# Performance work log

Measured on AMD Instinct MI355X. Metric: run time of the kernel, lower is better.

Reference implementation:

```python
import jax, jax.numpy as jnp
import numpy as np

N_FILTERS = 8   # K
N_SIMPLICES = 8192  # N (rows/cols of Laplacian)
BATCH = 64      # B
FEAT = 128      # F

def setup_inputs() -> dict:
    key = jax.random.key(0)
    k1, k2, k3 = jax.random.split(key, 3)
    x = jax.random.normal(k1, (BATCH, N_SIMPLICES, FEAT), dtype=jnp.float32)
    L = jax.random.normal(k2, (N_SIMPLICES, N_SIMPLICES), dtype=jnp.float32)
    # filter_weights: K vectors of length N, init N(0, 0.01) in the original
    W = 0.01 * jax.random.normal(k3, (N_FILTERS, N_SIMPLICES), dtype=jnp.float32)
    return {"x": x, "L": L, "W": W}

def reference(x, L, W):
    # Original per filter k: act( sum_n w_k[n] * (L @ x[b])[n, f] )
    # = act( (w_k^T L) @ x[b] ).  Fuse diag(w)@Lx + sum into wL = W @ L.
    wL = jnp.matmul(W, L)                       # [K, N]
    out = jnp.einsum('kn,bnf->kbf', wL, x)      # [K, B, F]
    return jnp.tanh(out)                        # stacked version of the K-output list
```

## Files before the change

kernel.cpp:

```cpp
#include <hip/hip_runtime.h>
#include <math.h>

#define N_SIMP 8192
#define K_FILT 8
#define BATCH  64
#define FEAT   128
#define MCHUNK 64
#define NCHUNK 64


__global__ __launch_bounds__(256) void wl_partial_kernel(const float* __restrict__ W,
                                                         const float* __restrict__ L,
                                                         float* __restrict__ pL) {
    const int ntile = blockIdx.x & 7;
    const int mc    = blockIdx.x >> 3;
    const int n0    = ntile * 1024;
    const int m0    = mc * 128;

    __shared__ float Ws[K_FILT][128];
    for (int idx = threadIdx.x; idx < K_FILT * 128; idx += 256) {
        int k = idx >> 7, j = idx & 127;
        Ws[k][j] = W[k * N_SIMP + m0 + j];
    }
    __syncthreads();

    const int n = n0 + threadIdx.x * 4;
    float4 acc[K_FILT];
#pragma unroll
    for (int k = 0; k < K_FILT; k++) acc[k] = make_float4(0.f, 0.f, 0.f, 0.f);

    const float* Lp = L + (size_t)m0 * N_SIMP + n;
    for (int j0 = 0; j0 < 128; j0 += 4) {
        float4 l0 = *(const float4*)(Lp);
        float4 l1 = *(const float4*)(Lp + N_SIMP);
        float4 l2 = *(const float4*)(Lp + 2 * N_SIMP);
        float4 l3 = *(const float4*)(Lp + 3 * N_SIMP);
        Lp += 4 * N_SIMP;
#pragma unroll
        for (int k = 0; k < K_FILT; k++) {
            float w0 = Ws[k][j0], w1 = Ws[k][j0 + 1], w2 = Ws[k][j0 + 2], w3 = Ws[k][j0 + 3];
            acc[k].x += w0 * l0.x; acc[k].y += w0 * l0.y; acc[k].z += w0 * l0.z; acc[k].w += w0 * l0.w;
            acc[k].x += w1 * l1.x; acc[k].y += w1 * l1.y; acc[k].z += w1 * l1.z; acc[k].w += w1 * l1.w;
            acc[k].x += w2 * l2.x; acc[k].y += w2 * l2.y; acc[k].z += w2 * l2.z; acc[k].w += w2 * l2.w;
            acc[k].x += w3 * l3.x; acc[k].y += w3 * l3.y; acc[k].z += w3 * l3.z; acc[k].w += w3 * l3.w;
        }
    }

#pragma unroll
    for (int k = 0; k < K_FILT; k++)
        *(float4*)&pL[(size_t)(mc * K_FILT + k) * N_SIMP + n] = acc[k];
}

__global__ __launch_bounds__(256) void wl_reduce_kernel(const float* __restrict__ pL,
                                                        float* __restrict__ wL) {
    const int i4 = (blockIdx.x * 256 + threadIdx.x) * 4;
    float4 s = make_float4(0.f, 0.f, 0.f, 0.f);
#pragma unroll 4
    for (int mc = 0; mc < MCHUNK; mc++) {
        float4 v = *(const float4*)&pL[(size_t)mc * (K_FILT * N_SIMP) + i4];
        s.x += v.x; s.y += v.y; s.z += v.z; s.w += v.w;
    }
    *(float4*)&wL[i4] = s;
}

__global__ __launch_bounds__(64) void conv_partial_kernel(const float* __restrict__ wL,
                                                          const float* __restrict__ x,
                                                          float* __restrict__ pO) {
    const int nc   = blockIdx.x & 63;
    const int b    = blockIdx.x >> 6;
    const int n0   = nc * 128;
    const int lane = threadIdx.x;
    const int f0   = (lane & 31) * 4;
    const int nl   = lane >> 5;

    __shared__ float wls[K_FILT][128];
    for (int idx = lane; idx < K_FILT * 128; idx += 64) {
        int k = idx >> 7, j = idx & 127;
        wls[k][j] = wL[k * N_SIMP + n0 + j];
    }
    __syncthreads();

    float4 acc[K_FILT];
#pragma unroll
    for (int k = 0; k < K_FILT; k++) acc[k] = make_float4(0.f, 0.f, 0.f, 0.f);

    const float* xp = x + (size_t)b * N_SIMP * FEAT + (size_t)(n0 + nl) * FEAT + f0;
    for (int j0 = 0; j0 < 128; j0 += 8) {
        float4 x0 = *(const float4*)(xp);
        float4 x1 = *(const float4*)(xp + 2 * FEAT);
        float4 x2 = *(const float4*)(xp + 4 * FEAT);
        float4 x3 = *(const float4*)(xp + 6 * FEAT);
        xp += 8 * FEAT;
#pragma unroll
        for (int k = 0; k < K_FILT; k++) {
            float w0 = wls[k][j0 + 0 + nl];
            float w1 = wls[k][j0 + 2 + nl];
            float w2 = wls[k][j0 + 4 + nl];
            float w3 = wls[k][j0 + 6 + nl];
            acc[k].x += w0 * x0.x; acc[k].y += w0 * x0.y; acc[k].z += w0 * x0.z; acc[k].w += w0 * x0.w;
            acc[k].x += w1 * x1.x; acc[k].y += w1 * x1.y; acc[k].z += w1 * x1.z; acc[k].w += w1 * x1.w;
            acc[k].x += w2 * x2.x; acc[k].y += w2 * x2.y; acc[k].z += w2 * x2.z; acc[k].w += w2 * x2.w;
            acc[k].x += w3 * x3.x; acc[k].y += w3 * x3.y; acc[k].z += w3 * x3.z; acc[k].w += w3 * x3.w;
        }
    }

#pragma unroll
    for (int k = 0; k < K_FILT; k++) {
        acc[k].x += __shfl_xor(acc[k].x, 32);
        acc[k].y += __shfl_xor(acc[k].y, 32);
        acc[k].z += __shfl_xor(acc[k].z, 32);
        acc[k].w += __shfl_xor(acc[k].w, 32);
    }

    if (nl == 0) {
#pragma unroll
        for (int k = 0; k < K_FILT; k++)
            *(float4*)&pO[((size_t)(nc * K_FILT + k) * BATCH + b) * FEAT + f0] = acc[k];
    }
}

__global__ __launch_bounds__(256) void conv_reduce_kernel(const float* __restrict__ pO,
                                                          float* __restrict__ out) {
    const int i4 = (blockIdx.x * 256 + threadIdx.x) * 4;
    float4 s = make_float4(0.f, 0.f, 0.f, 0.f);
#pragma unroll 4
    for (int nc = 0; nc < NCHUNK; nc++) {
        float4 v = *(const float4*)&pO[(size_t)nc * (K_FILT * BATCH * FEAT) + i4];
        s.x += v.x; s.y += v.y; s.z += v.z; s.w += v.w;
    }
    float4 r;
    r.x = tanhf(s.x); r.y = tanhf(s.y); r.z = tanhf(s.z); r.w = tanhf(s.w);
    *(float4*)&out[i4] = r;
}

__global__ void zero_ws_kernel(float* __restrict__ p, int n) {
    int i = blockIdx.x * blockDim.x + threadIdx.x;
    if (i < n) p[i] = 0.0f;
}

__global__ __launch_bounds__(256) void wl_atomic_kernel(const float* __restrict__ W,
                                                        const float* __restrict__ L,
                                                        float* __restrict__ wL) {
    const int ntile = blockIdx.x & 7;
    const int mc    = blockIdx.x >> 3;
    const int n0    = ntile * 1024;
    const int m0    = mc * 128;
    __shared__ float Ws[K_FILT][128];
    for (int idx = threadIdx.x; idx < K_FILT * 128; idx += 256) {
        int k = idx >> 7, j = idx & 127;
        Ws[k][j] = W[k * N_SIMP + m0 + j];
    }
    __syncthreads();
    const int n = n0 + threadIdx.x * 4;
    float4 acc[K_FILT];
#pragma unroll
    for (int k = 0; k < K_FILT; k++) acc[k] = make_float4(0.f, 0.f, 0.f, 0.f);
    const float* Lp = L + (size_t)m0 * N_SIMP + n;
    for (int j = 0; j < 128; j++) {
        float4 lv = *(const float4*)Lp;
        Lp += N_SIMP;
#pragma unroll
        for (int k = 0; k < K_FILT; k++) {
            float w = Ws[k][j];
            acc[k].x += w * lv.x; acc[k].y += w * lv.y; acc[k].z += w * lv.z; acc[k].w += w * lv.w;
        }
    }
#pragma unroll
    for (int k = 0; k < K_FILT; k++) {
        float* dst = &wL[k * N_SIMP + n];
        atomicAdd(dst + 0, acc[k].x); atomicAdd(dst + 1, acc[k].y);
        atomicAdd(dst + 2, acc[k].z); atomicAdd(dst + 3, acc[k].w);
    }
}

__global__ __launch_bounds__(64) void conv_atomic_kernel(const float* __restrict__ wL,
                                                         const float* __restrict__ x,
                                                         float* __restrict__ out_acc) {
    const int nc   = blockIdx.x & 63;
    const int b    = blockIdx.x >> 6;
    const int n0   = nc * 128;
    const int lane = threadIdx.x;
    const int f0   = (lane & 31) * 4;
    const int nl   = lane >> 5;
    __shared__ float wls[K_FILT][128];
    for (int idx = lane; idx < K_FILT * 128; idx += 64) {
        int k = idx >> 7, j = idx & 127;
        wls[k][j] = wL[k * N_SIMP + n0 + j];
    }
    __syncthreads();
    float4 acc[K_FILT];
#pragma unroll
    for (int k = 0; k < K_FILT; k++) acc[k] = make_float4(0.f, 0.f, 0.f, 0.f);
    const float* xp = x + (size_t)b * N_SIMP * FEAT + (size_t)(n0 + nl) * FEAT + f0;
    for (int jj = 0; jj < 64; jj++) {
        int j = jj * 2 + nl;
        float4 xv = *(const float4*)xp;
        xp += 2 * FEAT;
#pragma unroll
        for (int k = 0; k < K_FILT; k++) {
            float w = wls[k][j];
            acc[k].x += w * xv.x; acc[k].y += w * xv.y; acc[k].z += w * xv.z; acc[k].w += w * xv.w;
        }
    }
#pragma unroll
    for (int k = 0; k < K_FILT; k++) {
        acc[k].x += __shfl_xor(acc[k].x, 32);
        acc[k].y += __shfl_xor(acc[k].y, 32);
        acc[k].z += __shfl_xor(acc[k].z, 32);
        acc[k].w += __shfl_xor(acc[k].w, 32);
    }
    if (nl == 0) {
#pragma unroll
        for (int k = 0; k < K_FILT; k++) {
            float* dst = &out_acc[((size_t)k * BATCH + b) * FEAT + f0];
            atomicAdd(dst + 0, acc[k].x); atomicAdd(dst + 1, acc[k].y);
            atomicAdd(dst + 2, acc[k].z); atomicAdd(dst + 3, acc[k].w);
        }
    }
}

__global__ void tanh_kernel(const float* __restrict__ acc, float* __restrict__ out) {
    int i = blockIdx.x * blockDim.x + threadIdx.x;
    if (i < K_FILT * BATCH * FEAT) out[i] = tanhf(acc[i]);
}

extern "C" void kernel_launch(void* const* d_in, const int* in_sizes, int n_in,
                              void* d_out, int out_size, void* d_ws, size_t ws_size,
                              hipStream_t stream) {
    const float* x = (const float*)d_in[0];
    const float* L = (const float*)d_in[1];
    const float* W = (const float*)d_in[2];
    float* out = (float*)d_out;

    const size_t partial_elems = (size_t)MCHUNK * K_FILT * N_SIMP;
    const size_t need = (partial_elems + K_FILT * N_SIMP) * sizeof(float);

    if (ws_size >= need) {
        float* partials = (float*)d_ws;
        float* wL       = partials + partial_elems;

        wl_partial_kernel<<<8 * MCHUNK, 256, 0, stream>>>(W, L, partials);
        wl_reduce_kernel<<<64, 256, 0, stream>>>(partials, wL);
        conv_partial_kernel<<<BATCH * NCHUNK, 64, 0, stream>>>(wL, x, partials);
        conv_reduce_kernel<<<64, 256, 0, stream>>>(partials, out);
    } else {
        float* wL      = (float*)d_ws;
        float* out_acc = wL + (size_t)K_FILT * N_SIMP;
        const int n_zero = K_FILT * N_SIMP + K_FILT * BATCH * FEAT;
        zero_ws_kernel<<<(n_zero + 255) / 256, 256, 0, stream>>>(wL, n_zero);
        wl_atomic_kernel<<<512, 256, 0, stream>>>(W, L, wL);
        conv_atomic_kernel<<<BATCH * 64, 64, 0, stream>>>(wL, x, out_acc);
        tanh_kernel<<<(K_FILT * BATCH * FEAT + 255) / 256, 256, 0, stream>>>(out_acc, out);
    }
}
```

Baseline: 516.3 us.

## Software-prefetch L and x loads and split reductions across more blocks

The wL partial kernel now loads eight rows of L at a time and prefetches the next eight while computing on the current ones. The conv partial kernel gets the same double-buffered prefetch of x rows. Both reduction kernels are replaced by one templated reduce that splits the 64 partial chunks across four thread groups per block, combines them through shared memory, and launches 256 blocks instead of 64 to raise parallelism. The prefetching raises register pressure, which may lower occupancy.

```diff
diff --git a/kernel.cpp b/kernel.cpp
--- a/kernel.cpp
+++ b/kernel.cpp
@@ -30,19 +30,37 @@
     for (int k = 0; k < K_FILT; k++) acc[k] = make_float4(0.f, 0.f, 0.f, 0.f);
 
     const float* Lp = L + (size_t)m0 * N_SIMP + n;
-    for (int j0 = 0; j0 < 128; j0 += 4) {
-        float4 l0 = *(const float4*)(Lp);
-        float4 l1 = *(const float4*)(Lp + N_SIMP);
-        float4 l2 = *(const float4*)(Lp + 2 * N_SIMP);
-        float4 l3 = *(const float4*)(Lp + 3 * N_SIMP);
-        Lp += 4 * N_SIMP;
-#pragma unroll
-        for (int k = 0; k < K_FILT; k++) {
-            float w0 = Ws[k][j0], w1 = Ws[k][j0 + 1], w2 = Ws[k][j0 + 2], w3 = Ws[k][j0 + 3];
-            acc[k].x += w0 * l0.x; acc[k].y += w0 * l0.y; acc[k].z += w0 * l0.z; acc[k].w += w0 * l0.w;
-            acc[k].x += w1 * l1.x; acc[k].y += w1 * l1.y; acc[k].z += w1 * l1.z; acc[k].w += w1 * l1.w;
-            acc[k].x += w2 * l2.x; acc[k].y += w2 * l2.y; acc[k].z += w2 * l2.z; acc[k].w += w2 * l2.w;
-            acc[k].x += w3 * l3.x; acc[k].y += w3 * l3.y; acc[k].z += w3 * l3.z; acc[k].w += w3 * l3.w;
+
+    float4 c[8];
+#pragma unroll
+    for (int r = 0; r < 8; r++) c[r] = *(const float4*)(Lp + (size_t)r * N_SIMP);
+    Lp += 8 * (size_t)N_SIMP;
+
+    for (int j0 = 0; j0 < 120; j0 += 8) {
+        float4 nx[8];
+#pragma unroll
+        for (int r = 0; r < 8; r++) nx[r] = *(const float4*)(Lp + (size_t)r * N_SIMP);
+        Lp += 8 * (size_t)N_SIMP;
+
+#pragma unroll
+        for (int k = 0; k < K_FILT; k++) {
+#pragma unroll
+            for (int r = 0; r < 8; r++) {
+                float w = Ws[k][j0 + r];
+                acc[k].x += w * c[r].x; acc[k].y += w * c[r].y;
+                acc[k].z += w * c[r].z; acc[k].w += w * c[r].w;
+            }
+        }
+#pragma unroll
+        for (int r = 0; r < 8; r++) c[r] = nx[r];
+    }
+#pragma unroll
+    for (int k = 0; k < K_FILT; k++) {
+#pragma unroll
+        for (int r = 0; r < 8; r++) {
+            float w = Ws[k][120 + r];
+            acc[k].x += w * c[r].x; acc[k].y += w * c[r].y;
+            acc[k].z += w * c[r].z; acc[k].w += w * c[r].w;
         }
     }
 
@@ -51,16 +69,36 @@
         *(float4*)&pL[(size_t)(mc * K_FILT + k) * N_SIMP + n] = acc[k];
 }
 
-__global__ __launch_bounds__(256) void wl_reduce_kernel(const float* __restrict__ pL,
-                                                        float* __restrict__ wL) {
-    const int i4 = (blockIdx.x * 256 + threadIdx.x) * 4;
+template <bool TANH>
+__global__ __launch_bounds__(256) void reduce64_kernel(const float* __restrict__ p,
+                                                       float* __restrict__ out) {
+    const int t  = threadIdx.x & 63;
+    const int g  = threadIdx.x >> 6;
+    const int i4 = blockIdx.x * 256 + t * 4;
+
+    const float* base = p + (size_t)(g * 16) * 65536 + i4;
     float4 s = make_float4(0.f, 0.f, 0.f, 0.f);
-#pragma unroll 4
-    for (int mc = 0; mc < MCHUNK; mc++) {
-        float4 v = *(const float4*)&pL[(size_t)mc * (K_FILT * N_SIMP) + i4];
+#pragma unroll
+    for (int mc = 0; mc < 16; mc++) {
+        float4 v = *(const float4*)(base + (size_t)mc * 65536);
         s.x += v.x; s.y += v.y; s.z += v.z; s.w += v.w;
     }
-    *(float4*)&wL[i4] = s;
+
+    __shared__ float4 red[4][64];
+    red[g][t] = s;
+    __syncthreads();
+
+    if (g == 0) {
+        float4 a = red[1][t], b = red[2][t], c = red[3][t];
+        s.x += a.x + b.x + c.x;
+        s.y += a.y + b.y + c.y;
+        s.z += a.z + b.z + c.z;
+        s.w += a.w + b.w + c.w;
+        if (TANH) {
+            s.x = tanhf(s.x); s.y = tanhf(s.y); s.z = tanhf(s.z); s.w = tanhf(s.w);
+        }
+        *(float4*)&out[i4] = s;
+    }
 }
 
 __global__ __launch_bounds__(64) void conv_partial_kernel(const float* __restrict__ wL,
@@ -84,13 +122,8 @@
 #pragma unroll
     for (int k = 0; k < K_FILT; k++) acc[k] = make_float4(0.f, 0.f, 0.f, 0.f);
 
-    const float* xp = x + (size_t)b * N_SIMP * FEAT + (size_t)(n0 + nl) * FEAT + f0;
-    for (int j0 = 0; j0 < 128; j0 += 8) {
-        float4 x0 = *(const float4*)(xp);
-        float4 x1 = *(const float4*)(xp + 2 * FEAT);
-        float4 x2 = *(const float4*)(xp + 4 * FEAT);
-        float4 x3 = *(const float4*)(xp + 6 * FEAT);
-        xp += 8 * FEAT;
+    auto compute = [&](int j0, const float4& x0, const float4& x1,
+                       const float4& x2, const float4& x3) {
 #pragma unroll
         for (int k = 0; k < K_FILT; k++) {
             float w0 = wls[k][j0 + 0 + nl];
@@ -102,7 +135,25 @@
             acc[k].x += w2 * x2.x; acc[k].y += w2 * x2.y; acc[k].z += w2 * x2.z; acc[k].w += w2 * x2.w;
             acc[k].x += w3 * x3.x; acc[k].y += w3 * x3.y; acc[k].z += w3 * x3.z; acc[k].w += w3 * x3.w;
         }
-    }
+    };
+
+    const float* xp = x + (size_t)b * N_SIMP * FEAT + (size_t)(n0 + nl) * FEAT + f0;
+    float4 c0 = *(const float4*)(xp);
+    float4 c1 = *(const float4*)(xp + 2 * FEAT);
+    float4 c2 = *(const float4*)(xp + 4 * FEAT);
+    float4 c3 = *(const float4*)(xp + 6 * FEAT);
+    xp += 8 * FEAT;
+
+    for (int j0 = 0; j0 < 120; j0 += 8) {
+        float4 p0 = *(const float4*)(xp);
+        float4 p1 = *(const float4*)(xp + 2 * FEAT);
+        float4 p2 = *(const float4*)(xp + 4 * FEAT);
+        float4 p3 = *(const float4*)(xp + 6 * FEAT);
+        xp += 8 * FEAT;
+        compute(j0, c0, c1, c2, c3);
+        c0 = p0; c1 = p1; c2 = p2; c3 = p3;
+    }
+    compute(120, c0, c1, c2, c3);
 
 #pragma unroll
     for (int k = 0; k < K_FILT; k++) {
@@ -117,20 +168,6 @@
         for (int k = 0; k < K_FILT; k++)
             *(float4*)&pO[((size_t)(nc * K_FILT + k) * BATCH + b) * FEAT + f0] = acc[k];
     }
-}
-
-__global__ __launch_bounds__(256) void conv_reduce_kernel(const float* __restrict__ pO,
-                                                          float* __restrict__ out) {
-    const int i4 = (blockIdx.x * 256 + threadIdx.x) * 4;
-    float4 s = make_float4(0.f, 0.f, 0.f, 0.f);
-#pragma unroll 4
-    for (int nc = 0; nc < NCHUNK; nc++) {
-        float4 v = *(const float4*)&pO[(size_t)nc * (K_FILT * BATCH * FEAT) + i4];
-        s.x += v.x; s.y += v.y; s.z += v.z; s.w += v.w;
-    }
-    float4 r;
-    r.x = tanhf(s.x); r.y = tanhf(s.y); r.z = tanhf(s.z); r.w = tanhf(s.w);
-    *(float4*)&out[i4] = r;
 }
 
 __global__ void zero_ws_kernel(float* __restrict__ p, int n) {
@@ -240,9 +277,9 @@
         float* wL       = partials + partial_elems;
 
         wl_partial_kernel<<<8 * MCHUNK, 256, 0, stream>>>(W, L, partials);
-        wl_reduce_kernel<<<64, 256, 0, stream>>>(partials, wL);
+        reduce64_kernel<false><<<256, 256, 0, stream>>>(partials, wL);
         conv_partial_kernel<<<BATCH * NCHUNK, 64, 0, stream>>>(wL, x, partials);
-        conv_reduce_kernel<<<64, 256, 0, stream>>>(partials, out);
+        reduce64_kernel<true><<<256, 256, 0, stream>>>(partials, out);
     } else {
         float* wL      = (float*)d_ws;
         float* out_acc = wL + (size_t)K_FILT * N_SIMP;
```

Measured after the change: 517.0 us. No clear change (+0.1%).
